# Optimization experiments

Measured on AMD Instinct MI355X. Metric: run time of the kernel, lower is better.

Reference implementation:

```python
import jax, jax.numpy as jnp
import numpy as np

D_MODEL = 1024
NUM_EXPERTS = 8
TOP_K = 2


def setup_inputs() -> dict:
    key = jax.random.key(0)
    ks = jax.random.split(key, 8)
    d, e = D_MODEL, NUM_EXPERTS
    s = 0.02
    return {
        "x": jax.random.normal(ks[0], (2, 2048, d), dtype=jnp.float32),
        "router_w": jax.random.normal(ks[1], (d, e), dtype=jnp.float32) * s,
        "router_b": jnp.zeros((e,), dtype=jnp.float32),
        "w1": jax.random.normal(ks[2], (e, d, 4 * d), dtype=jnp.float32) * s,
        "b1": jnp.zeros((e, 4 * d), dtype=jnp.float32),
        "w2": jax.random.normal(ks[3], (e, 4 * d, d), dtype=jnp.float32) * s,
        "b2": jnp.zeros((e, d), dtype=jnp.float32),
    }


def reference(x, router_w, router_b, w1, b1, w2, b2):
    orig_shape = x.shape
    d = x.shape[-1]
    xf = x.reshape(-1, d)                      # [T, d]
    T = xf.shape[0]

    logits = xf @ router_w + router_b          # [T, E]
    probs = jax.nn.softmax(logits, axis=-1)    # [T, E]
    top_v, top_i = jax.lax.top_k(probs, TOP_K)  # [T, k]
    top_v = top_v / jnp.sum(top_v, axis=-1, keepdims=True)

    # dense combine weights, zero except the top-k experts per token
    comb = jnp.zeros_like(probs).at[jnp.arange(T)[:, None], top_i].add(top_v)  # [T, E]

    # run every expert on every token (dense grouped GEMM), then weighted combine
    h = jax.nn.gelu(jnp.einsum("td,edf->etf", xf, w1) + b1[:, None, :], approximate=False)  # [E, T, 4d]
    y = jnp.einsum("etf,efd->etd", h, w2) + b2[:, None, :]                                   # [E, T, d]
    out = jnp.einsum("te,etd->td", comb, y)                                                   # [T, d]

    mean_probs = probs.mean(axis=0)
    aux_loss = jnp.var(mean_probs, ddof=1)     # torch.var default is unbiased
    return out.reshape(orig_shape), aux_loss
```

## Files before the change

kernel.cpp:

```cpp
#include <hip/hip_runtime.h>


#define TOKENS 4096
#define DMODEL 1024
#define NEXP   8
#define DFF    4096
#define NROWS  (2*TOKENS)
#define SPLITK 4

typedef __bf16 bf16_t;
typedef __bf16 bf16x8 __attribute__((ext_vector_type(8)));
typedef __bf16 bf16x4 __attribute__((ext_vector_type(4)));
typedef float  f32x4  __attribute__((ext_vector_type(4)));

__device__ __forceinline__ void gl_lds16(const void* g, void* l) {
    __builtin_amdgcn_global_load_lds(
        (const __attribute__((address_space(1))) void*)g,
        (__attribute__((address_space(3))) void*)l, 16, 0, 0);
}

__global__ __launch_bounds__(64) void router_k(
    const float* __restrict__ x, const float* __restrict__ rw,
    const float* __restrict__ rb, int* __restrict__ cnt,
    int* __restrict__ tok_e, int* __restrict__ tok_pos,
    float* __restrict__ tok_w, float* __restrict__ probs,
    bf16_t* __restrict__ xb)
{
    int t = blockIdx.x;
    int lane = threadIdx.x;
    const float* xr = x + (size_t)t * DMODEL;
    bf16_t* xbr = xb + (size_t)t * DMODEL;
    float s[NEXP];
#pragma unroll
    for (int e = 0; e < NEXP; e++) s[e] = 0.f;
    for (int i = lane; i < DMODEL; i += 64) {
        float xv = xr[i];
        xbr[i] = (bf16_t)xv;
        const float* wr = rw + (size_t)i * NEXP;
#pragma unroll
        for (int e = 0; e < NEXP; e++) s[e] += xv * wr[e];
    }
#pragma unroll
    for (int e = 0; e < NEXP; e++) {
#pragma unroll
        for (int o = 32; o > 0; o >>= 1) s[e] += __shfl_down(s[e], o, 64);
    }
    if (lane == 0) {
        float mx = -1e30f;
#pragma unroll
        for (int e = 0; e < NEXP; e++) { s[e] += rb[e]; mx = fmaxf(mx, s[e]); }
        float den = 0.f;
#pragma unroll
        for (int e = 0; e < NEXP; e++) { s[e] = expf(s[e] - mx); den += s[e]; }
        float inv = 1.f / den;
#pragma unroll
        for (int e = 0; e < NEXP; e++) { s[e] *= inv; probs[t * NEXP + e] = s[e]; }
        int e0 = 0;
#pragma unroll
        for (int e = 1; e < NEXP; e++) if (s[e] > s[e0]) e0 = e;
        int e1 = (e0 == 0) ? 1 : 0;
#pragma unroll
        for (int e = 0; e < NEXP; e++) if (e != e0 && s[e] > s[e1]) e1 = e;
        float sw = s[e0] + s[e1];
        int p0 = atomicAdd(&cnt[e0], 1);
        int p1 = atomicAdd(&cnt[e1], 1);
        tok_e[2 * t] = e0;       tok_e[2 * t + 1] = e1;
        tok_pos[2 * t] = p0;     tok_pos[2 * t + 1] = p1;
        tok_w[2 * t] = s[e0] / sw; tok_w[2 * t + 1] = s[e1] / sw;
    }
}

__global__ void offsets_k(const int* __restrict__ cnt, int* __restrict__ off)
{
    if (threadIdx.x == 0) {
        int a = 0;
        for (int e = 0; e < NEXP; e++) { off[e] = a; a += cnt[e]; }
        off[NEXP] = a;
    }
}

__global__ void scatter_k(const int* __restrict__ tok_e, const int* __restrict__ tok_pos,
                          const float* __restrict__ tok_w, const int* __restrict__ off,
                          int* __restrict__ rows_tok, float* __restrict__ roww,
                          int* __restrict__ g_of)
{
    int i = blockIdx.x * blockDim.x + threadIdx.x;
    if (i < 2 * TOKENS) {
        int e = tok_e[i];
        int g = off[e] + tok_pos[i];
        rows_tok[g] = i >> 1;
        roww[g] = tok_w[i];
        g_of[i] = g;
    }
}

#define TP 65
__global__ __launch_bounds__(256) void transconv_k(const float* __restrict__ in,
                                                   bf16_t* __restrict__ o, int K, int N)
{
    __shared__ float t[64 * TP];
    int e = blockIdx.z;
    int n0 = blockIdx.x * 64, k0 = blockIdx.y * 64;
    int tid = threadIdx.x;
    int c4 = tid & 15, r = tid >> 4;
    const float* src = in + ((size_t)e * K + k0) * N + n0;
#pragma unroll
    for (int p = 0; p < 4; p++) {
        int k = r + p * 16;
        float4 v = *(const float4*)(src + (size_t)k * N + c4 * 4);
        float* d = &t[k * TP + c4 * 4];
        d[0] = v.x; d[1] = v.y; d[2] = v.z; d[3] = v.w;
    }
    __syncthreads();
    int k8 = tid & 7, n = tid >> 3;
    bf16_t* dst = o + ((size_t)e * N + n0) * K + k0;
#pragma unroll
    for (int p = 0; p < 2; p++) {
        int nn = n + p * 32;
        bf16x8 w;
#pragma unroll
        for (int j = 0; j < 8; j++) w[j] = (bf16_t)t[(k8 * 8 + j) * TP + nn];
        *(bf16x8*)(dst + (size_t)nn * K + k8 * 8) = w;
    }
}

__global__ __launch_bounds__(256, 2) void gemm1_k(
    const bf16_t* __restrict__ A, const bf16_t* __restrict__ Bt,
    const float* __restrict__ bias,
    const int* __restrict__ cnt, const int* __restrict__ off,
    const int* __restrict__ rows_tok, bf16_t* __restrict__ hbuf)
{
    int bid = blockIdx.x;
    int e = bid & 7;
    int rest = bid >> 3;
    int yt = rest & 31;
    int xt = rest >> 5;
    int M = cnt[e];
    int m0 = yt * 128;
    if (m0 >= M) return;
    int n0 = xt * 128;
    int base = off[e];

    __shared__ __align__(16) bf16_t lA[128 * 64];
    __shared__ __align__(16) bf16_t lB[128 * 64];

    int tid = threadIdx.x;
    int wave = tid >> 6;
    int lane = tid & 63;
    int sc = (lane & 7) ^ (lane >> 3);

    const bf16_t* aRow[4];
    const bf16_t* bRow[4];
#pragma unroll
    for (int i = 0; i < 4; i++) {
        int r = (wave * 4 + i) * 8 + (lane >> 3);
        int gr = m0 + r; if (gr > M - 1) gr = M - 1;
        int tok = rows_tok[base + gr];
        aRow[i] = A + (size_t)tok * DMODEL;
        bRow[i] = Bt + ((size_t)e * DFF + n0 + r) * DMODEL;
    }

    f32x4 acc[4][4];
    f32x4 zero = { 0.f, 0.f, 0.f, 0.f };
#pragma unroll
    for (int i = 0; i < 4; i++)
#pragma unroll
        for (int j = 0; j < 4; j++) acc[i][j] = zero;

    int wrow = wave >> 1, wcol = wave & 1;

#pragma unroll 1
    for (int kk = 0; kk < DMODEL / 64; ++kk) {
        int koff = kk * 64 + sc * 8;
#pragma unroll
        for (int i = 0; i < 4; i++) {
            gl_lds16(aRow[i] + koff, &lA[(wave * 4 + i) * 512]);
            gl_lds16(bRow[i] + koff, &lB[(wave * 4 + i) * 512]);
        }
        __syncthreads();
#pragma unroll
        for (int ks = 0; ks < 2; ++ks) {
            bf16x8 af[4], bfr[4];
#pragma unroll
            for (int mt = 0; mt < 4; mt++) {
                int r = wrow * 64 + mt * 16 + (lane & 15);
                int ch = (ks * 4 + (lane >> 4)) ^ (r & 7);
                af[mt] = *(const bf16x8*)&lA[r * 64 + ch * 8];
            }
#pragma unroll
            for (int nt = 0; nt < 4; nt++) {
                int c = wcol * 64 + nt * 16 + (lane & 15);
                int ch = (ks * 4 + (lane >> 4)) ^ (c & 7);
                bfr[nt] = *(const bf16x8*)&lB[c * 64 + ch * 8];
            }
#pragma unroll
            for (int mt = 0; mt < 4; mt++)
#pragma unroll
                for (int nt = 0; nt < 4; nt++)
                    acc[mt][nt] = __builtin_amdgcn_mfma_f32_16x16x32_bf16(
                        af[mt], bfr[nt], acc[mt][nt], 0, 0, 0);
        }
        __syncthreads();
    }

    float bv[4];
#pragma unroll
    for (int nt = 0; nt < 4; nt++)
        bv[nt] = bias[(size_t)e * DFF + n0 + wcol * 64 + nt * 16 + (lane & 15)];

#pragma unroll
    for (int mt = 0; mt < 4; mt++) {
#pragma unroll
        for (int q = 0; q < 4; q++) {
            int r = wrow * 64 + mt * 16 + (lane >> 4) * 4 + q;
            int gm = m0 + r;
            if (gm < M) {
                size_t hrow = (size_t)(base + gm) * DFF;
#pragma unroll
                for (int nt = 0; nt < 4; nt++) {
                    float v = acc[mt][nt][q] + bv[nt];
                    v = 0.5f * v * (1.f + erff(v * 0.70710678118654752f));
                    int c = n0 + wcol * 64 + nt * 16 + (lane & 15);
                    hbuf[hrow + c] = (bf16_t)v;
                }
            }
        }
    }
}

__global__ __launch_bounds__(256, 2) void gemm2_k(
    const bf16_t* __restrict__ A, const bf16_t* __restrict__ Bt,
    const int* __restrict__ cnt, const int* __restrict__ off,
    bf16_t* __restrict__ ybuf)
{
    int bid = blockIdx.x;
    int e = bid & 7;
    int rest = bid >> 3;
    int yt = rest & 31;
    int xt = (rest >> 5) & 7;
    int kt = rest >> 8;
    int M = cnt[e];
    int m0 = yt * 128;
    if (m0 >= M) return;
    int n0 = xt * 128;
    int base = off[e];
    int k0 = kt * (DFF / SPLITK);

    __shared__ __align__(16) bf16_t lA[128 * 64];
    __shared__ __align__(16) bf16_t lB[128 * 64];

    int tid = threadIdx.x;
    int wave = tid >> 6;
    int lane = tid & 63;
    int sc = (lane & 7) ^ (lane >> 3);

    const bf16_t* aRow[4];
    const bf16_t* bRow[4];
#pragma unroll
    for (int i = 0; i < 4; i++) {
        int r = (wave * 4 + i) * 8 + (lane >> 3);
        int gr = m0 + r; if (gr > M - 1) gr = M - 1;
        aRow[i] = A + (size_t)(base + gr) * DFF + k0;
        bRow[i] = Bt + ((size_t)e * DMODEL + n0 + r) * DFF + k0;
    }

    f32x4 acc[4][4];
    f32x4 zero = { 0.f, 0.f, 0.f, 0.f };
#pragma unroll
    for (int i = 0; i < 4; i++)
#pragma unroll
        for (int j = 0; j < 4; j++) acc[i][j] = zero;

    int wrow = wave >> 1, wcol = wave & 1;

#pragma unroll 1
    for (int kk = 0; kk < (DFF / SPLITK) / 64; ++kk) {
        int koff = kk * 64 + sc * 8;
#pragma unroll
        for (int i = 0; i < 4; i++) {
            gl_lds16(aRow[i] + koff, &lA[(wave * 4 + i) * 512]);
            gl_lds16(bRow[i] + koff, &lB[(wave * 4 + i) * 512]);
        }
        __syncthreads();
#pragma unroll
        for (int ks = 0; ks < 2; ++ks) {
            bf16x8 af[4], bfr[4];
#pragma unroll
            for (int mt = 0; mt < 4; mt++) {
                int r = wrow * 64 + mt * 16 + (lane & 15);
                int ch = (ks * 4 + (lane >> 4)) ^ (r & 7);
                af[mt] = *(const bf16x8*)&lA[r * 64 + ch * 8];
            }
#pragma unroll
            for (int nt = 0; nt < 4; nt++) {
                int c = wcol * 64 + nt * 16 + (lane & 15);
                int ch = (ks * 4 + (lane >> 4)) ^ (c & 7);
                bfr[nt] = *(const bf16x8*)&lB[c * 64 + ch * 8];
            }
#pragma unroll
            for (int mt = 0; mt < 4; mt++)
#pragma unroll
                for (int nt = 0; nt < 4; nt++)
                    acc[mt][nt] = __builtin_amdgcn_mfma_f32_16x16x32_bf16(
                        af[mt], bfr[nt], acc[mt][nt], 0, 0, 0);
        }
        __syncthreads();
    }

#pragma unroll
    for (int mt = 0; mt < 4; mt++) {
#pragma unroll
        for (int q = 0; q < 4; q++) {
            int r = wrow * 64 + mt * 16 + (lane >> 4) * 4 + q;
            int gm = m0 + r;
            if (gm < M) {
                size_t yrow = ((size_t)kt * NROWS + base + gm) * DMODEL;
#pragma unroll
                for (int nt = 0; nt < 4; nt++) {
                    int c = n0 + wcol * 64 + nt * 16 + (lane & 15);
                    ybuf[yrow + c] = (bf16_t)acc[mt][nt][q];
                }
            }
        }
    }
}

__global__ __launch_bounds__(256) void combine_k(
    const bf16_t* __restrict__ ybuf, const int* __restrict__ g_of,
    const int* __restrict__ tok_e, const float* __restrict__ tok_w,
    const float* __restrict__ b2, float* __restrict__ out)
{
    int t = blockIdx.x;
    int c = threadIdx.x * 4;
    int g0 = g_of[2 * t], g1 = g_of[2 * t + 1];
    int e0 = tok_e[2 * t], e1 = tok_e[2 * t + 1];
    float w0 = tok_w[2 * t], w1 = tok_w[2 * t + 1];
    float a0[4] = {0.f, 0.f, 0.f, 0.f}, a1[4] = {0.f, 0.f, 0.f, 0.f};
#pragma unroll
    for (int kt = 0; kt < SPLITK; kt++) {
        bf16x4 y0 = *(const bf16x4*)&ybuf[((size_t)kt * NROWS + g0) * DMODEL + c];
        bf16x4 y1 = *(const bf16x4*)&ybuf[((size_t)kt * NROWS + g1) * DMODEL + c];
#pragma unroll
        for (int j = 0; j < 4; j++) { a0[j] += (float)y0[j]; a1[j] += (float)y1[j]; }
    }
    float4 bb0 = *(const float4*)&b2[(size_t)e0 * DMODEL + c];
    float4 bb1 = *(const float4*)&b2[(size_t)e1 * DMODEL + c];
    float4 r;
    r.x = w0 * (a0[0] + bb0.x) + w1 * (a1[0] + bb1.x);
    r.y = w0 * (a0[1] + bb0.y) + w1 * (a1[1] + bb1.y);
    r.z = w0 * (a0[2] + bb0.z) + w1 * (a1[2] + bb1.z);
    r.w = w0 * (a0[3] + bb0.w) + w1 * (a1[3] + bb1.w);
    *(float4*)&out[(size_t)t * DMODEL + c] = r;
}

__global__ __launch_bounds__(256) void aux_k(const float* __restrict__ probs,
                                             float* __restrict__ out_aux)
{
    __shared__ float red[256];
    __shared__ float mexp[NEXP];
    float s[NEXP];
#pragma unroll
    for (int e = 0; e < NEXP; e++) s[e] = 0.f;
    for (int t = threadIdx.x; t < TOKENS; t += 256) {
#pragma unroll
        for (int e = 0; e < NEXP; e++) s[e] += probs[t * NEXP + e];
    }
    for (int e = 0; e < NEXP; e++) {
        red[threadIdx.x] = s[e];
        __syncthreads();
        for (int st = 128; st > 0; st >>= 1) {
            if (threadIdx.x < st) red[threadIdx.x] += red[threadIdx.x + st];
            __syncthreads();
        }
        if (threadIdx.x == 0) mexp[e] = red[0] / (float)TOKENS;
        __syncthreads();
    }
    if (threadIdx.x == 0) {
        float mean = 0.f;
        for (int e = 0; e < NEXP; e++) mean += mexp[e];
        mean /= (float)NEXP;
        float v = 0.f;
        for (int e = 0; e < NEXP; e++) { float d = mexp[e] - mean; v += d * d; }
        out_aux[0] = v / (float)(NEXP - 1);
    }
}

extern "C" void kernel_launch(void* const* d_in, const int* in_sizes, int n_in,
                              void* d_out, int out_size, void* d_ws, size_t ws_size,
                              hipStream_t stream)
{
    const float* x  = (const float*)d_in[0];
    const float* rw = (const float*)d_in[1];
    const float* rb = (const float*)d_in[2];
    const float* w1 = (const float*)d_in[3];
    const float* b1 = (const float*)d_in[4];
    const float* w2 = (const float*)d_in[5];
    const float* b2 = (const float*)d_in[6];
    float* out = (float*)d_out;

    char* p = (char*)d_ws;
    auto alloc = [&](size_t b) { char* q = p; p += (b + 255) & ~(size_t)255; return q; };
    int*    cnt      = (int*)   alloc(NEXP * sizeof(int));
    int*    off      = (int*)   alloc((NEXP + 1) * sizeof(int));
    int*    tok_e    = (int*)   alloc(2 * TOKENS * sizeof(int));
    int*    tok_pos  = (int*)   alloc(2 * TOKENS * sizeof(int));
    float*  tok_w    = (float*) alloc(2 * TOKENS * sizeof(float));
    int*    rows_tok = (int*)   alloc(NROWS * sizeof(int));
    float*  roww     = (float*) alloc(NROWS * sizeof(float));
    int*    g_of     = (int*)   alloc(2 * TOKENS * sizeof(int));
    float*  probs    = (float*) alloc((size_t)TOKENS * NEXP * sizeof(float));
    bf16_t* xb       = (bf16_t*)alloc((size_t)TOKENS * DMODEL * 2);
    bf16_t* w1t      = (bf16_t*)alloc((size_t)NEXP * DFF * DMODEL * 2);
    bf16_t* w2t      = (bf16_t*)alloc((size_t)NEXP * DMODEL * DFF * 2);
    bf16_t* hbuf     = (bf16_t*)alloc((size_t)NROWS * DFF * 2);
    bf16_t* ybuf     = w1t;

    hipMemsetAsync(cnt, 0, NEXP * sizeof(int), stream);

    router_k<<<TOKENS, 64, 0, stream>>>(x, rw, rb, cnt, tok_e, tok_pos, tok_w, probs, xb);
    offsets_k<<<1, 64, 0, stream>>>(cnt, off);
    scatter_k<<<(2 * TOKENS + 255) / 256, 256, 0, stream>>>(tok_e, tok_pos, tok_w, off,
                                                            rows_tok, roww, g_of);
    transconv_k<<<dim3(DFF / 64, DMODEL / 64, NEXP), 256, 0, stream>>>(w1, w1t, DMODEL, DFF);
    transconv_k<<<dim3(DMODEL / 64, DFF / 64, NEXP), 256, 0, stream>>>(w2, w2t, DFF, DMODEL);

    gemm1_k<<<NEXP * 32 * 32, 256, 0, stream>>>(xb, w1t, b1, cnt, off, rows_tok, hbuf);
    gemm2_k<<<NEXP * 32 * 8 * SPLITK, 256, 0, stream>>>(hbuf, w2t, cnt, off, ybuf);
    combine_k<<<TOKENS, 256, 0, stream>>>(ybuf, g_of, tok_e, tok_w, b2, out);

    aux_k<<<1, 256, 0, stream>>>(probs, out + (size_t)TOKENS * DMODEL);
}
```

Measured before the change: 657.9 us.

## Merge expert GEMMs into a 256x256-tile double-buffered 8-phase pipelined kernel

Replaces the two separate 128x128 grouped GEMM kernels with one templated kernel. It uses 256x256 tiles, 512 threads and two LDS buffers. Global-to-LDS loads for upcoming K tiles are interleaved across eight MFMA phases, with explicit vmcnt waits, raw barriers and s_setprio. The aim is to hide memory latency behind matrix math and raise arithmetic intensity per block. The costs are heavy LDS use (128KB, so about one block per CU), more padded-row waste on uneven expert counts, and a fragile hand-written wait/barrier schedule.

Result: slower. 730.0 us (+10.9%).

```diff
diff --git a/kernel.cpp b/kernel.cpp
--- a/kernel.cpp
+++ b/kernel.cpp
@@ -124,201 +124,177 @@
     }
 }
 
-__global__ __launch_bounds__(256, 2) void gemm1_k(
+
+#define STG_A(BUF, J, KK) gl_lds16(arow[J] + (KK) * 64 + sc8, &(BUF)[(J) * 4096 + wave * 512])
+#define STG_B(BUF, J, KK) gl_lds16(brow[J] + (KK) * 64 + sc8, &(BUF)[(J) * 4096 + wave * 512])
+#define W6 asm volatile("s_waitcnt vmcnt(6)" ::: "memory")
+#define W0 asm volatile("s_waitcnt vmcnt(0)" ::: "memory")
+#define NOSTG (void)0
+#define NOWAIT (void)0
+
+#define PH(LA, LB, P, STAGE, WAIT)                                              \
+  do {                                                                          \
+    bf16x8 af_[2][2];                                                           \
+    _Pragma("unroll")                                                           \
+    for (int dm_ = 0; dm_ < 2; dm_++) {                                         \
+        int r_ = wrow * 128 + (2 * (P) + dm_) * 16 + (lane & 15);               \
+        _Pragma("unroll")                                                       \
+        for (int ks_ = 0; ks_ < 2; ks_++) {                                     \
+            int ch_ = (ks_ * 4 + (lane >> 4)) ^ (r_ & 7);                       \
+            af_[dm_][ks_] = *(const bf16x8*)&(LA)[r_ * 64 + ch_ * 8];           \
+        }                                                                       \
+    }                                                                           \
+    if ((P) == 0) {                                                             \
+        _Pragma("unroll")                                                       \
+        for (int nt_ = 0; nt_ < 4; nt_++) {                                     \
+            int c_ = wcol * 64 + nt_ * 16 + (lane & 15);                        \
+            _Pragma("unroll")                                                   \
+            for (int ks_ = 0; ks_ < 2; ks_++) {                                 \
+                int ch_ = (ks_ * 4 + (lane >> 4)) ^ (c_ & 7);                   \
+                bfr[nt_][ks_] = *(const bf16x8*)&(LB)[c_ * 64 + ch_ * 8];       \
+            }                                                                   \
+        }                                                                       \
+    }                                                                           \
+    STAGE;                                                                      \
+    __builtin_amdgcn_s_barrier();                                               \
+    asm volatile("s_waitcnt lgkmcnt(0)" ::: "memory");                          \
+    __builtin_amdgcn_s_setprio(1);                                              \
+    _Pragma("unroll")                                                           \
+    for (int dm_ = 0; dm_ < 2; dm_++)                                           \
+        _Pragma("unroll")                                                       \
+        for (int nt_ = 0; nt_ < 4; nt_++)                                       \
+            _Pragma("unroll")                                                   \
+            for (int ks_ = 0; ks_ < 2; ks_++)                                   \
+                acc[2 * (P) + dm_][nt_] = __builtin_amdgcn_mfma_f32_16x16x32_bf16( \
+                    af_[dm_][ks_], bfr[nt_][ks_], acc[2 * (P) + dm_][nt_], 0, 0, 0); \
+    __builtin_amdgcn_s_setprio(0);                                              \
+    WAIT;                                                                       \
+    __builtin_amdgcn_s_barrier();                                               \
+  } while (0)
+
+template <int MODE>
+__global__ __launch_bounds__(512, 2) void gemm8p_k(
     const bf16_t* __restrict__ A, const bf16_t* __restrict__ Bt,
     const float* __restrict__ bias,
     const int* __restrict__ cnt, const int* __restrict__ off,
-    const int* __restrict__ rows_tok, bf16_t* __restrict__ hbuf)
+    const int* __restrict__ rows_tok, bf16_t* __restrict__ outb)
 {
     int bid = blockIdx.x;
     int e = bid & 7;
     int rest = bid >> 3;
-    int yt = rest & 31;
-    int xt = rest >> 5;
+    int yt = rest & 15;
+    int xt, kt;
+    if (MODE == 0) { xt = rest >> 4; kt = 0; }
+    else           { xt = (rest >> 4) & 3; kt = rest >> 6; }
     int M = cnt[e];
-    int m0 = yt * 128;
+    int m0 = yt * 256;
     if (m0 >= M) return;
-    int n0 = xt * 128;
+    int n0 = xt * 256;
     int base = off[e];
-
-    __shared__ __align__(16) bf16_t lA[128 * 64];
-    __shared__ __align__(16) bf16_t lB[128 * 64];
+    const int k0 = (MODE == 0) ? 0 : kt * (DFF / SPLITK);
+
+    __shared__ __align__(16) bf16_t lds[4 * 16384];
+    bf16_t* lA0 = lds;
+    bf16_t* lB0 = lds + 16384;
+    bf16_t* lA1 = lds + 32768;
+    bf16_t* lB1 = lds + 49152;
 
     int tid = threadIdx.x;
     int wave = tid >> 6;
     int lane = tid & 63;
-    int sc = (lane & 7) ^ (lane >> 3);
-
-    const bf16_t* aRow[4];
-    const bf16_t* bRow[4];
-#pragma unroll
-    for (int i = 0; i < 4; i++) {
-        int r = (wave * 4 + i) * 8 + (lane >> 3);
-        int gr = m0 + r; if (gr > M - 1) gr = M - 1;
-        int tok = rows_tok[base + gr];
-        aRow[i] = A + (size_t)tok * DMODEL;
-        bRow[i] = Bt + ((size_t)e * DFF + n0 + r) * DMODEL;
-    }
-
-    f32x4 acc[4][4];
+    int wrow = wave >> 2;
+    int wcol = wave & 3;
+    int srow = tid >> 3;
+    int sc8 = ((tid & 7) ^ (srow & 7)) * 8;
+
+    const bf16_t* arow[4];
+    const bf16_t* brow[4];
+#pragma unroll
+    for (int j = 0; j < 4; j++) {
+        int gr = m0 + j * 64 + srow; if (gr > M - 1) gr = M - 1;
+        if (MODE == 0) {
+            int tok = rows_tok[base + gr];
+            arow[j] = A + (size_t)tok * DMODEL;
+            brow[j] = Bt + ((size_t)e * DFF + n0 + j * 64 + srow) * DMODEL;
+        } else {
+            arow[j] = A + (size_t)(base + gr) * DFF + k0;
+            brow[j] = Bt + ((size_t)e * DMODEL + n0 + j * 64 + srow) * DFF + k0;
+        }
+    }
+
+    f32x4 acc[8][4];
     f32x4 zero = { 0.f, 0.f, 0.f, 0.f };
 #pragma unroll
-    for (int i = 0; i < 4; i++)
+    for (int i = 0; i < 8; i++)
 #pragma unroll
         for (int j = 0; j < 4; j++) acc[i][j] = zero;
-
-    int wrow = wave >> 1, wcol = wave & 1;
+    bf16x8 bfr[4][2];
+
+    STG_B(lB0, 0, 0); STG_B(lB0, 1, 0); STG_B(lB0, 2, 0); STG_B(lB0, 3, 0);
+    STG_A(lA0, 0, 0); STG_A(lA0, 1, 0); STG_A(lA0, 2, 0); STG_A(lA0, 3, 0);
+    STG_B(lB1, 0, 1); STG_B(lB1, 1, 1); STG_B(lB1, 2, 1); STG_B(lB1, 3, 1);
+    STG_A(lA1, 0, 1); STG_A(lA1, 2, 1);
+    W6;
+    __builtin_amdgcn_s_barrier();
 
 #pragma unroll 1
-    for (int kk = 0; kk < DMODEL / 64; ++kk) {
-        int koff = kk * 64 + sc * 8;
-#pragma unroll
-        for (int i = 0; i < 4; i++) {
-            gl_lds16(aRow[i] + koff, &lA[(wave * 4 + i) * 512]);
-            gl_lds16(bRow[i] + koff, &lB[(wave * 4 + i) * 512]);
-        }
-        __syncthreads();
-#pragma unroll
-        for (int ks = 0; ks < 2; ++ks) {
-            bf16x8 af[4], bfr[4];
-#pragma unroll
-            for (int mt = 0; mt < 4; mt++) {
-                int r = wrow * 64 + mt * 16 + (lane & 15);
-                int ch = (ks * 4 + (lane >> 4)) ^ (r & 7);
-                af[mt] = *(const bf16x8*)&lA[r * 64 + ch * 8];
-            }
-#pragma unroll
-            for (int nt = 0; nt < 4; nt++) {
-                int c = wcol * 64 + nt * 16 + (lane & 15);
-                int ch = (ks * 4 + (lane >> 4)) ^ (c & 7);
-                bfr[nt] = *(const bf16x8*)&lB[c * 64 + ch * 8];
-            }
-#pragma unroll
-            for (int mt = 0; mt < 4; mt++)
-#pragma unroll
-                for (int nt = 0; nt < 4; nt++)
-                    acc[mt][nt] = __builtin_amdgcn_mfma_f32_16x16x32_bf16(
-                        af[mt], bfr[nt], acc[mt][nt], 0, 0, 0);
-        }
-        __syncthreads();
-    }
-
-    float bv[4];
-#pragma unroll
-    for (int nt = 0; nt < 4; nt++)
-        bv[nt] = bias[(size_t)e * DFF + n0 + wcol * 64 + nt * 16 + (lane & 15)];
-
-#pragma unroll
-    for (int mt = 0; mt < 4; mt++) {
-#pragma unroll
-        for (int q = 0; q < 4; q++) {
-            int r = wrow * 64 + mt * 16 + (lane >> 4) * 4 + q;
-            int gm = m0 + r;
-            if (gm < M) {
-                size_t hrow = (size_t)(base + gm) * DFF;
-#pragma unroll
-                for (int nt = 0; nt < 4; nt++) {
-                    float v = acc[mt][nt][q] + bv[nt];
-                    v = 0.5f * v * (1.f + erff(v * 0.70710678118654752f));
-                    int c = n0 + wcol * 64 + nt * 16 + (lane & 15);
-                    hbuf[hrow + c] = (bf16_t)v;
+    for (int i = 0; i < 7; i++) {
+        int tO1 = 2 * i + 1, tE2 = 2 * i + 2, tO3 = 2 * i + 3;
+        PH(lA0, lB0, 0, { STG_A(lA1, 1, tO1); STG_A(lA1, 3, tO1); }, NOWAIT);
+        PH(lA0, lB0, 1, { STG_B(lB0, 0, tE2); STG_B(lB0, 1, tE2); }, NOWAIT);
+        PH(lA0, lB0, 2, { STG_B(lB0, 2, tE2); STG_B(lB0, 3, tE2); STG_A(lA0, 0, tE2); }, NOWAIT);
+        PH(lA0, lB0, 3, { STG_A(lA0, 2, tE2); }, W6);
+        PH(lA1, lB1, 0, { STG_A(lA0, 1, tE2); STG_A(lA0, 3, tE2); }, NOWAIT);
+        PH(lA1, lB1, 1, { STG_B(lB1, 0, tO3); STG_B(lB1, 1, tO3); }, NOWAIT);
+        PH(lA1, lB1, 2, { STG_B(lB1, 2, tO3); STG_B(lB1, 3, tO3); STG_A(lA1, 0, tO3); }, NOWAIT);
+        PH(lA1, lB1, 3, { STG_A(lA1, 2, tO3); }, W6);
+    }
+    PH(lA0, lB0, 0, { STG_A(lA1, 1, 15); STG_A(lA1, 3, 15); }, NOWAIT);
+    PH(lA0, lB0, 1, NOSTG, NOWAIT);
+    PH(lA0, lB0, 2, NOSTG, NOWAIT);
+    PH(lA0, lB0, 3, NOSTG, W0);
+    PH(lA1, lB1, 0, NOSTG, NOWAIT);
+    PH(lA1, lB1, 1, NOSTG, NOWAIT);
+    PH(lA1, lB1, 2, NOSTG, NOWAIT);
+    PH(lA1, lB1, 3, NOSTG, NOWAIT);
+
+    if (MODE == 0) {
+        float bv[4];
+#pragma unroll
+        for (int nt = 0; nt < 4; nt++)
+            bv[nt] = bias[(size_t)e * DFF + n0 + wcol * 64 + nt * 16 + (lane & 15)];
+#pragma unroll
+        for (int mt = 0; mt < 8; mt++) {
+#pragma unroll
+            for (int q = 0; q < 4; q++) {
+                int r = wrow * 128 + mt * 16 + (lane >> 4) * 4 + q;
+                int gm = m0 + r;
+                if (gm < M) {
+                    size_t hrow = (size_t)(base + gm) * DFF;
+#pragma unroll
+                    for (int nt = 0; nt < 4; nt++) {
+                        float v = acc[mt][nt][q] + bv[nt];
+                        v = 0.5f * v * (1.f + erff(v * 0.70710678118654752f));
+                        int c = n0 + wcol * 64 + nt * 16 + (lane & 15);
+                        outb[hrow + c] = (bf16_t)v;
+                    }
                 }
             }
         }
-    }
-}
-
-__global__ __launch_bounds__(256, 2) void gemm2_k(
-    const bf16_t* __restrict__ A, const bf16_t* __restrict__ Bt,
-    const int* __restrict__ cnt, const int* __restrict__ off,
-    bf16_t* __restrict__ ybuf)
-{
-    int bid = blockIdx.x;
-    int e = bid & 7;
-    int rest = bid >> 3;
-    int yt = rest & 31;
-    int xt = (rest >> 5) & 7;
-    int kt = rest >> 8;
-    int M = cnt[e];
-    int m0 = yt * 128;
-    if (m0 >= M) return;
-    int n0 = xt * 128;
-    int base = off[e];
-    int k0 = kt * (DFF / SPLITK);
-
-    __shared__ __align__(16) bf16_t lA[128 * 64];
-    __shared__ __align__(16) bf16_t lB[128 * 64];
-
-    int tid = threadIdx.x;
-    int wave = tid >> 6;
-    int lane = tid & 63;
-    int sc = (lane & 7) ^ (lane >> 3);
-
-    const bf16_t* aRow[4];
-    const bf16_t* bRow[4];
-#pragma unroll
-    for (int i = 0; i < 4; i++) {
-        int r = (wave * 4 + i) * 8 + (lane >> 3);
-        int gr = m0 + r; if (gr > M - 1) gr = M - 1;
-        aRow[i] = A + (size_t)(base + gr) * DFF + k0;
-        bRow[i] = Bt + ((size_t)e * DMODEL + n0 + r) * DFF + k0;
-    }
-
-    f32x4 acc[4][4];
-    f32x4 zero = { 0.f, 0.f, 0.f, 0.f };
-#pragma unroll
-    for (int i = 0; i < 4; i++)
-#pragma unroll
-        for (int j = 0; j < 4; j++) acc[i][j] = zero;
-
-    int wrow = wave >> 1, wcol = wave & 1;
-
-#pragma unroll 1
-    for (int kk = 0; kk < (DFF / SPLITK) / 64; ++kk) {
-        int koff = kk * 64 + sc * 8;
-#pragma unroll
-        for (int i = 0; i < 4; i++) {
-            gl_lds16(aRow[i] + koff, &lA[(wave * 4 + i) * 512]);
-            gl_lds16(bRow[i] + koff, &lB[(wave * 4 + i) * 512]);
-        }
-        __syncthreads();
-#pragma unroll
-        for (int ks = 0; ks < 2; ++ks) {
-            bf16x8 af[4], bfr[4];
-#pragma unroll
-            for (int mt = 0; mt < 4; mt++) {
-                int r = wrow * 64 + mt * 16 + (lane & 15);
-                int ch = (ks * 4 + (lane >> 4)) ^ (r & 7);
-                af[mt] = *(const bf16x8*)&lA[r * 64 + ch * 8];
-            }
-#pragma unroll
-            for (int nt = 0; nt < 4; nt++) {
-                int c = wcol * 64 + nt * 16 + (lane & 15);
-                int ch = (ks * 4 + (lane >> 4)) ^ (c & 7);
-                bfr[nt] = *(const bf16x8*)&lB[c * 64 + ch * 8];
-            }
-#pragma unroll
-            for (int mt = 0; mt < 4; mt++)
-#pragma unroll
-                for (int nt = 0; nt < 4; nt++)
-                    acc[mt][nt] = __builtin_amdgcn_mfma_f32_16x16x32_bf16(
-                        af[mt], bfr[nt], acc[mt][nt], 0, 0, 0);
-        }
-        __syncthreads();
-    }
-
-#pragma unroll
-    for (int mt = 0; mt < 4; mt++) {
-#pragma unroll
-        for (int q = 0; q < 4; q++) {
-            int r = wrow * 64 + mt * 16 + (lane >> 4) * 4 + q;
-            int gm = m0 + r;
-            if (gm < M) {
-                size_t yrow = ((size_t)kt * NROWS + base + gm) * DMODEL;
-#pragma unroll
-                for (int nt = 0; nt < 4; nt++) {
-                    int c = n0 + wcol * 64 + nt * 16 + (lane & 15);
-                    ybuf[yrow + c] = (bf16_t)acc[mt][nt][q];
+    } else {
+#pragma unroll
+        for (int mt = 0; mt < 8; mt++) {
+#pragma unroll
+            for (int q = 0; q < 4; q++) {
+                int r = wrow * 128 + mt * 16 + (lane >> 4) * 4 + q;
+                int gm = m0 + r;
+                if (gm < M) {
+                    size_t yrow = ((size_t)kt * NROWS + base + gm) * DMODEL;
+#pragma unroll
+                    for (int nt = 0; nt < 4; nt++) {
+                        int c = n0 + wcol * 64 + nt * 16 + (lane & 15);
+                        outb[yrow + c] = (bf16_t)acc[mt][nt][q];
+                    }
                 }
             }
         }
@@ -424,8 +400,9 @@
     transconv_k<<<dim3(DFF / 64, DMODEL / 64, NEXP), 256, 0, stream>>>(w1, w1t, DMODEL, DFF);
     transconv_k<<<dim3(DMODEL / 64, DFF / 64, NEXP), 256, 0, stream>>>(w2, w2t, DFF, DMODEL);
 
-    gemm1_k<<<NEXP * 32 * 32, 256, 0, stream>>>(xb, w1t, b1, cnt, off, rows_tok, hbuf);
-    gemm2_k<<<NEXP * 32 * 8 * SPLITK, 256, 0, stream>>>(hbuf, w2t, cnt, off, ybuf);
+    gemm8p_k<0><<<NEXP * 16 * 16, 512, 0, stream>>>(xb, w1t, b1, cnt, off, rows_tok, hbuf);
+    gemm8p_k<1><<<NEXP * 16 * 4 * SPLITK, 512, 0, stream>>>(hbuf, w2t, nullptr, cnt, off,
+                                                            nullptr, ybuf);
     combine_k<<<TOKENS, 256, 0, stream>>>(ybuf, g_of, tok_e, tok_w, b2, out);
 
     aux_k<<<1, 256, 0, stream>>>(probs, out + (size_t)TOKENS * DMODEL);
```
